# Optimization experiments

Measured on AMD Instinct MI355X. Metric: run time of the kernel, lower is better.

The kernel has to match this reference:

```python
import jax, jax.numpy as jnp
import numpy as np

# Module constants from init_kwargs
A, T, HID, H, EGO = 50, 50, 128, 32, 0
C = 4 * HID // H   # per-head out channels = 16
B = 32
NEG_SLOPE = 0.2    # PyG GATConv default negative_slope


def setup_inputs() -> dict:
    key = jax.random.key(0)
    k1, k2, k3, k4 = jax.random.split(key, 4)
    h = jax.random.normal(k1, (B, A, T, HID), dtype=jnp.float32)
    # GATConv params: lin.weight (H*C, HID), att_src/att_dst (H, C), bias (H*C,)
    W = jax.random.normal(k2, (H * C, HID), dtype=jnp.float32) * (1.0 / np.sqrt(HID))
    att_src = jax.random.normal(k3, (H, C), dtype=jnp.float32) * 0.1
    att_dst = jax.random.normal(k4, (H, C), dtype=jnp.float32) * 0.1
    bias = jnp.zeros((H * C,), dtype=jnp.float32)
    return {"h": h, "W": W, "att_src": att_src, "att_dst": att_dst, "bias": bias}


def reference(h, W, att_src, att_dst, bias):
    # h: (B, A, T, HID). Node id = t*A + a after permute, matching build_ego_star_edges.
    b = h.shape[0]
    x = jnp.transpose(h, (0, 2, 1, 3))                       # (B, T, A, HID)
    # Linear projection into heads: (B, T, A, H, C)
    xw = jnp.einsum('btad,hcd->btahc', x, W.reshape(H, C, HID))
    a_src = jnp.einsum('btahc,hc->btah', xw, att_src)        # per-node src logit
    a_dst = jnp.einsum('btahc,hc->btah', xw, att_dst)        # per-node dst logit

    # Star topology: every (t_src, a != EGO) node -> every (t_dst, EGO) node.
    ne = jnp.array([a for a in range(A) if a != EGO])        # (A-1,) non-ego agents
    S = T * (A - 1)                                          # neighbors per ego dst
    x_ne = xw[:, :, ne].reshape(b, S, H, C)                  # (B, S, H, C)
    a_src_ne = a_src[:, :, ne].reshape(b, S, H)              # (B, S, H)
    a_dst_ego = a_dst[:, :, EGO]                             # (B, T, H)

    # Per-edge attention logits, segment-softmax over the S neighbors of each dst.
    logits = jax.nn.leaky_relu(a_src_ne[:, None, :, :] + a_dst_ego[:, :, None, :],
                               negative_slope=NEG_SLOPE)     # (B, T, S, H)
    att = jax.nn.softmax(logits, axis=2)

    # Weighted aggregation: (B, T, H, C) -> flatten heads (concat=True)
    out_ego = jnp.einsum('btsh,bshc->bthc', att, x_ne).reshape(b, T, H * C)

    # Nodes with no incoming edges get zero aggregation; bias added to all.
    out = jnp.zeros((b, T, A, H * C), dtype=h.dtype).at[:, :, EGO].set(out_ego)
    out = out + bias
    return jnp.transpose(out, (0, 2, 1, 3))                  # (B, A, T, H*C)
```

## Files before the change

kernel.cpp:

```cpp
#include <hip/hip_runtime.h>
#include <math.h>

#define NA    50
#define NT    50
#define HIDK  128
#define NH    32
#define NC    16
#define NB    32
#define SAT   2500
#define NS    2450
#define NOUT  512

__global__ __launch_bounds__(256) void k_fill(const float* __restrict__ bias,
                                              float* __restrict__ out) {
  size_t i = (size_t)blockIdx.x * 256 + threadIdx.x;
  float4 b4 = ((const float4*)bias)[i & 127];
  ((float4*)out)[i] = b4;
}

__global__ __launch_bounds__(256) void k0_pq(const float* __restrict__ W,
                                             const float* __restrict__ att_src,
                                             const float* __restrict__ att_dst,
                                             float* __restrict__ PQ) {
  int g = blockIdx.x * 256 + threadIdx.x;
  int j = g >> 7, k = g & 127;
  int hh = j & 31;
  const float* att = (j < 32) ? att_src : att_dst;
  float acc = 0.f;
  #pragma unroll
  for (int c = 0; c < 16; ++c)
    acc = fmaf(att[hh * 16 + c], W[(size_t)(hh * 16 + c) * 128 + k], acc);
  PQ[g] = acc;
}

__global__ __launch_bounds__(256) void k1_ud(
    const float* __restrict__ X,
    const float* __restrict__ PQ,
    float* __restrict__ u,
    float* __restrict__ dv)
{
  __shared__ float Ast[32][68];
  __shared__ float Bst[32][68];
  const int tid = threadIdx.x;
  const int m0 = blockIdx.x * 64;
  const int ty = tid >> 4, tx = tid & 15;
  float acc[4][4] = {};
  const int sr = tid >> 3, sc = tid & 7;

  for (int kc = 0; kc < 128; kc += 32) {
    #pragma unroll
    for (int L = 0; L < 2; ++L) {
      int row = sr + L * 32;
      float4 v = *(const float4*)&X[(size_t)(m0 + row) * 128 + kc + sc * 4];
      Ast[sc*4+0][row] = v.x; Ast[sc*4+1][row] = v.y;
      Ast[sc*4+2][row] = v.z; Ast[sc*4+3][row] = v.w;
      float4 w = *(const float4*)&PQ[(size_t)row * 128 + kc + sc * 4];
      Bst[sc*4+0][row] = w.x; Bst[sc*4+1][row] = w.y;
      Bst[sc*4+2][row] = w.z; Bst[sc*4+3][row] = w.w;
    }
    __syncthreads();
    #pragma unroll
    for (int k = 0; k < 32; ++k) {
      float4 a4 = *(const float4*)&Ast[k][ty * 4];
      float4 b4 = *(const float4*)&Bst[k][tx * 4];
      float a[4] = {a4.x, a4.y, a4.z, a4.w};
      float bb[4] = {b4.x, b4.y, b4.z, b4.w};
      #pragma unroll
      for (int i = 0; i < 4; ++i)
        #pragma unroll
        for (int j = 0; j < 4; ++j)
          acc[i][j] = fmaf(a[i], bb[j], acc[i][j]);
    }
    __syncthreads();
  }

  #pragma unroll
  for (int i = 0; i < 4; ++i) {
    int m = m0 + ty * 4 + i;
    int b = m / SAT, s = m - b * SAT;
    #pragma unroll
    for (int jj = 0; jj < 4; ++jj) {
      int col = tx * 4 + jj;
      if (col < 32)
        u[(size_t)(b * 32 + col) * SAT + s] = acc[i][jj];
      else if (s < NT)
        dv[(size_t)(b * 32 + col - 32) * NT + s] = acc[i][jj];
    }
  }
}

#define LOADG(B_, g_) do {                                                  \
    _Pragma("unroll")                                                       \
    for (int j = 0; j < 4; ++j) {                                           \
      int idx_ = base + 2 * ((g_) * 4 + j);                                 \
      e##B_[j] = sE[idx_]; s##B_[j] = sIdx[idx_];                           \
    }                                                                       \
    _Pragma("unroll")                                                       \
    for (int j = 0; j < 4; ++j)                                             \
      x##B_[j] = *(const float4*)(xb + (size_t)s##B_[j] * HIDK);            \
  } while (0)

#define COMPG(B_) do {                                                      \
    _Pragma("unroll")                                                       \
    for (int j = 0; j < 4; ++j) {                                           \
      float2 ee = e##B_[j]; float4 xx = x##B_[j];                           \
      a1[0]=fmaf(ee.x,xx.x,a1[0]); a1[1]=fmaf(ee.x,xx.y,a1[1]);             \
      a1[2]=fmaf(ee.x,xx.z,a1[2]); a1[3]=fmaf(ee.x,xx.w,a1[3]);             \
      a2[0]=fmaf(ee.y,xx.x,a2[0]); a2[1]=fmaf(ee.y,xx.y,a2[1]);             \
      a2[2]=fmaf(ee.y,xx.z,a2[2]); a2[3]=fmaf(ee.y,xx.w,a2[3]);             \
      z1 += ee.x; z2 += ee.y;                                               \
    }                                                                       \
  } while (0)

__global__ __launch_bounds__(512, 4) void k2_attn(
    const float* __restrict__ X,
    const float* __restrict__ u,
    const float* __restrict__ dv,
    const float* __restrict__ W,
    const float* __restrict__ bias,
    float* __restrict__ out)
{
  const int id = blockIdx.x;
  const int b  = (id & 7) + 8 * (id >> 8);
  const int h  = (id >> 3) & 31;
  const int tid = threadIdx.x;

  __shared__ float Bb[2][51][129];
  __shared__ float2 sE[NS];
  __shared__ unsigned short sIdx[NS];
  __shared__ float sTheta[50], sD[50], sF1[50], sF2[50];
  __shared__ int   sRank[50];
  __shared__ int   offs[52];
  __shared__ int   offCur[51];
  __shared__ float red[8];
  __shared__ float sMaxU;

  float* sU = &Bb[0][0][0];
  unsigned short* sBeta = (unsigned short*)&Bb[1][0][0];

  const size_t bh = (size_t)b * 32 + h;
  const float* uP = u + bh * SAT + NT;
  for (int i = tid; i < NS; i += 512) sU[i] = uP[i];
  if (tid < 50) sD[tid] = dv[bh * NT + tid];
  if (tid < 51) offCur[tid] = 0;
  __syncthreads();

  float mx = -1e30f;
  for (int i = tid; i < NS; i += 512) mx = fmaxf(mx, sU[i]);
  #pragma unroll
  for (int o = 32; o; o >>= 1) mx = fmaxf(mx, __shfl_xor(mx, o));
  if ((tid & 63) == 0) red[tid >> 6] = mx;
  __syncthreads();
  if (tid == 0) {
    float m2 = red[0];
    #pragma unroll
    for (int k = 1; k < 8; ++k) m2 = fmaxf(m2, red[k]);
    sMaxU = m2;
  }
  __syncthreads();
  const float maxU = sMaxU;

  if (tid < 50) {
    float th = -sD[tid];
    int r = 0;
    for (int t2 = 0; t2 < 50; ++t2) {
      float th2 = -sD[t2];
      r += (th2 < th) || (th2 == th && t2 < tid);
    }
    sRank[tid] = r;
    sTheta[r] = th;
    float x = maxU + sD[tid];
    float L = (x >= 0.f) ? x : 0.2f * x;
    sF1[tid] = __expf(x - L);
    sF2[tid] = __expf(0.2f * x - L);
  }
  __syncthreads();

  for (int i = tid; i < NS; i += 512) {
    float uu = sU[i];
    int lo = 0, hi = 50;
    while (lo < hi) { int mid = (lo + hi) >> 1; if (sTheta[mid] <= uu) lo = mid + 1; else hi = mid; }
    sBeta[i] = (unsigned short)lo;
    atomicAdd(&offCur[lo], 1);
  }
  __syncthreads();
  if (tid == 0) {
    int run = 0;
    for (int k = 0; k < 51; ++k) { int c = offCur[k]; offs[k] = run; run += c; }
    offs[51] = run;
  }
  __syncthreads();
  if (tid < 51) offCur[tid] = offs[tid];
  __syncthreads();

  for (int i = tid; i < NS; i += 512) {
    float uu = sU[i];
    int beta = sBeta[i];
    int pos = atomicAdd(&offCur[beta], 1);
    sE[pos] = make_float2(__expf(uu - maxU), __expf(0.2f * (uu - maxU)));
    sIdx[pos] = (unsigned short)(i + NT);
  }
  __syncthreads();

  {
    const int wave = tid >> 6;
    const int lane = tid & 63;
    const int slot = lane >> 5;
    const int cq   = lane & 31;
    const float* xb = X + (size_t)b * SAT * HIDK + cq * 4;

    for (int seg = wave; seg < 51; seg += 8) {
      const int i0 = offs[seg], i1 = offs[seg + 1];
      const int base = i0 + slot;
      int np = i1 - base;
      np = (np > 0) ? ((np + 1) >> 1) : 0;
      const int G = np >> 2;

      float a1[4] = {0.f, 0.f, 0.f, 0.f};
      float a2[4] = {0.f, 0.f, 0.f, 0.f};
      float z1 = 0.f, z2 = 0.f;

      float2 eA[4], eB[4]; int sA[4], sB[4]; float4 xA[4], xB[4];
      int g = 0;
      if (G) LOADG(A, 0);
      while (g + 2 <= G) {
        LOADG(B, g + 1);
        COMPG(A);
        if (g + 2 < G) LOADG(A, g + 2);
        COMPG(B);
        g += 2;
      }
      if (g < G) COMPG(A);
      for (int k = G * 4; k < np; ++k) {
        int idx = base + 2 * k;
        float2 ee = sE[idx];
        int ss = sIdx[idx];
        float4 xx = *(const float4*)(xb + (size_t)ss * HIDK);
        a1[0]=fmaf(ee.x,xx.x,a1[0]); a1[1]=fmaf(ee.x,xx.y,a1[1]);
        a1[2]=fmaf(ee.x,xx.z,a1[2]); a1[3]=fmaf(ee.x,xx.w,a1[3]);
        a2[0]=fmaf(ee.y,xx.x,a2[0]); a2[1]=fmaf(ee.y,xx.y,a2[1]);
        a2[2]=fmaf(ee.y,xx.z,a2[2]); a2[3]=fmaf(ee.y,xx.w,a2[3]);
        z1 += ee.x; z2 += ee.y;
      }

      #pragma unroll
      for (int j = 0; j < 4; ++j) {
        a1[j] += __shfl_xor(a1[j], 32);
        a2[j] += __shfl_xor(a2[j], 32);
      }
      z1 += __shfl_xor(z1, 32);
      z2 += __shfl_xor(z2, 32);
      if (slot == 0) {
        #pragma unroll
        for (int j = 0; j < 4; ++j) {
          Bb[0][seg][cq * 4 + j] = a1[j];
          Bb[1][seg][cq * 4 + j] = a2[j];
        }
        if (cq == 0) { Bb[0][seg][128] = z1; Bb[1][seg][128] = z2; }
      }
    }
  }
  __syncthreads();

  float* WshT = (float*)sE;
  const float* Wh = W + (size_t)h * 16 * 128;
  for (int v = tid; v < 2048; v += 512) {
    int k = v >> 4, cout = v & 15;
    WshT[k * 16 + cout] = Wh[(size_t)cout * 128 + k];
  }
  for (int task = tid; task < 258; task += 512) {
    int which = task >= 129;
    int c = task - which * 129;
    if (which == 0) {
      float run = 0.f;
      for (int k = 50; k >= 0; --k) { float tmp = Bb[0][k][c]; Bb[0][k][c] = run; run += tmp; }
    } else {
      float run = 0.f;
      for (int k = 0; k <= 50; ++k) { run += Bb[1][k][c]; Bb[1][k][c] = run; }
    }
  }
  __syncthreads();

  for (int task = tid; task < NT * NC; task += 512) {
    int t = task >> 4, cout = task & 15;
    int r = sRank[t];
    float F1 = sF1[t], F2 = sF2[t];
    float z = F1 * Bb[0][r][128] + F2 * Bb[1][r][128];
    const float* b1r = &Bb[0][r][0];
    const float* b2r = &Bb[1][r][0];
    float n1 = 0.f, n2 = 0.f;
    #pragma unroll 4
    for (int c = 0; c < 128; ++c) {
      float w = WshT[c * 16 + cout];
      n1 = fmaf(b1r[c], w, n1);
      n2 = fmaf(b2r[c], w, n2);
    }
    out[((size_t)b * SAT + t) * NOUT + h * 16 + cout] =
        (F1 * n1 + F2 * n2) / z + bias[h * 16 + cout];
  }
}

extern "C" void kernel_launch(void* const* d_in, const int* in_sizes, int n_in,
                              void* d_out, int out_size, void* d_ws, size_t ws_size,
                              hipStream_t stream) {
  const float* X       = (const float*)d_in[0];
  const float* Wm      = (const float*)d_in[1];
  const float* att_src = (const float*)d_in[2];
  const float* att_dst = (const float*)d_in[3];
  const float* bias    = (const float*)d_in[4];
  float* out = (float*)d_out;

  float* PQ = (float*)d_ws;
  float* u  = PQ + 64 * 128;
  float* dv = u + (size_t)NB * NH * SAT;

  hipLaunchKernelGGL(k_fill, dim3(40000), dim3(256), 0, stream, bias, out);
  hipLaunchKernelGGL(k0_pq, dim3(32), dim3(256), 0, stream, Wm, att_src, att_dst, PQ);
  hipLaunchKernelGGL(k1_ud, dim3(1250), dim3(256), 0, stream, X, PQ, u, dv);
  hipLaunchKernelGGL(k2_attn, dim3(1024), dim3(512), 0, stream,
                     X, u, dv, Wm, bias, out);
}
```

Baseline: 318.7 us.

## Split attention kernel into gather and output stages, fold bias fill into output

Splits the big attention kernel into two. The gather kernel keeps only the sorted edge weights in LDS, which allows more resident blocks, and writes the partial sums plus per-head auxiliaries to workspace. A second kernel reloads them, runs the prefix scans and projection, and also writes the bias into the non-ego output rows, which replaces the separate full-output fill kernel. The cost is an extra global round-trip for the partial buffers, one more launch, and a repeated binary search.

New measurement: 682.7 us. 114% more time.

```diff
diff --git a/kernel.cpp b/kernel.cpp
--- a/kernel.cpp
+++ b/kernel.cpp
@@ -11,12 +11,10 @@
 #define NS    2450
 #define NOUT  512
 
-__global__ __launch_bounds__(256) void k_fill(const float* __restrict__ bias,
-                                              float* __restrict__ out) {
-  size_t i = (size_t)blockIdx.x * 256 + threadIdx.x;
-  float4 b4 = ((const float4*)bias)[i & 127];
-  ((float4*)out)[i] = b4;
-}
+#define SEGW   132
+#define WHICHW (51 * SEGW)
+#define BHW    (2 * WHICHW)
+#define AUXW   160
 
 __global__ __launch_bounds__(256) void k0_pq(const float* __restrict__ W,
                                              const float* __restrict__ att_src,
@@ -112,36 +110,32 @@
     }                                                                       \
   } while (0)
 
-__global__ __launch_bounds__(512, 4) void k2_attn(
+__global__ __launch_bounds__(512, 8) void k2a_gather(
     const float* __restrict__ X,
     const float* __restrict__ u,
     const float* __restrict__ dv,
-    const float* __restrict__ W,
-    const float* __restrict__ bias,
-    float* __restrict__ out)
+    float* __restrict__ Bpart,
+    float* __restrict__ aux)
 {
   const int id = blockIdx.x;
   const int b  = (id & 7) + 8 * (id >> 8);
   const int h  = (id >> 3) & 31;
   const int tid = threadIdx.x;
-
-  __shared__ float Bb[2][51][129];
+  const int bh = b * 32 + h;
+
   __shared__ float2 sE[NS];
+  __shared__ float  sU[NS];
   __shared__ unsigned short sIdx[NS];
-  __shared__ float sTheta[50], sD[50], sF1[50], sF2[50];
+  __shared__ float sTheta[50], sD[50];
   __shared__ int   sRank[50];
   __shared__ int   offs[52];
   __shared__ int   offCur[51];
   __shared__ float red[8];
   __shared__ float sMaxU;
 
-  float* sU = &Bb[0][0][0];
-  unsigned short* sBeta = (unsigned short*)&Bb[1][0][0];
-
-  const size_t bh = (size_t)b * 32 + h;
-  const float* uP = u + bh * SAT + NT;
+  const float* uP = u + (size_t)bh * SAT + NT;
   for (int i = tid; i < NS; i += 512) sU[i] = uP[i];
-  if (tid < 50) sD[tid] = dv[bh * NT + tid];
+  if (tid < 50) sD[tid] = dv[(size_t)bh * NT + tid];
   if (tid < 51) offCur[tid] = 0;
   __syncthreads();
 
@@ -171,8 +165,10 @@
     sTheta[r] = th;
     float x = maxU + sD[tid];
     float L = (x >= 0.f) ? x : 0.2f * x;
-    sF1[tid] = __expf(x - L);
-    sF2[tid] = __expf(0.2f * x - L);
+    float* ax = aux + (size_t)bh * AUXW;
+    ax[tid]       = __expf(x - L);
+    ax[50 + tid]  = __expf(0.2f * x - L);
+    ax[100 + tid] = (float)r;
   }
   __syncthreads();
 
@@ -180,7 +176,6 @@
     float uu = sU[i];
     int lo = 0, hi = 50;
     while (lo < hi) { int mid = (lo + hi) >> 1; if (sTheta[mid] <= uu) lo = mid + 1; else hi = mid; }
-    sBeta[i] = (unsigned short)lo;
     atomicAdd(&offCur[lo], 1);
   }
   __syncthreads();
@@ -195,8 +190,9 @@
 
   for (int i = tid; i < NS; i += 512) {
     float uu = sU[i];
-    int beta = sBeta[i];
-    int pos = atomicAdd(&offCur[beta], 1);
+    int lo = 0, hi = 50;
+    while (lo < hi) { int mid = (lo + hi) >> 1; if (sTheta[mid] <= uu) lo = mid + 1; else hi = mid; }
+    int pos = atomicAdd(&offCur[lo], 1);
     sE[pos] = make_float2(__expf(uu - maxU), __expf(0.2f * (uu - maxU)));
     sIdx[pos] = (unsigned short)(i + NT);
   }
@@ -208,6 +204,7 @@
     const int slot = lane >> 5;
     const int cq   = lane & 31;
     const float* xb = X + (size_t)b * SAT * HIDK + cq * 4;
+    float* bp = Bpart + (size_t)bh * BHW;
 
     for (int seg = wave; seg < 51; seg += 8) {
       const int i0 = offs[seg], i1 = offs[seg + 1];
@@ -251,24 +248,57 @@
       z1 += __shfl_xor(z1, 32);
       z2 += __shfl_xor(z2, 32);
       if (slot == 0) {
-        #pragma unroll
-        for (int j = 0; j < 4; ++j) {
-          Bb[0][seg][cq * 4 + j] = a1[j];
-          Bb[1][seg][cq * 4 + j] = a2[j];
+        float4 st1 = {a1[0], a1[1], a1[2], a1[3]};
+        float4 st2 = {a2[0], a2[1], a2[2], a2[3]};
+        *(float4*)&bp[seg * SEGW + cq * 4] = st1;
+        *(float4*)&bp[WHICHW + seg * SEGW + cq * 4] = st2;
+        if (cq == 0) {
+          bp[seg * SEGW + 128] = z1;
+          bp[WHICHW + seg * SEGW + 128] = z2;
         }
-        if (cq == 0) { Bb[0][seg][128] = z1; Bb[1][seg][128] = z2; }
       }
     }
   }
-  __syncthreads();
-
-  float* WshT = (float*)sE;
-  const float* Wh = W + (size_t)h * 16 * 128;
-  for (int v = tid; v < 2048; v += 512) {
-    int k = v >> 4, cout = v & 15;
-    WshT[k * 16 + cout] = Wh[(size_t)cout * 128 + k];
-  }
-  for (int task = tid; task < 258; task += 512) {
+}
+
+__global__ __launch_bounds__(256) void k2b_out(
+    const float* __restrict__ Bpart, const float* __restrict__ aux,
+    const float* __restrict__ W, const float* __restrict__ bias,
+    float* __restrict__ out)
+{
+  const int h = blockIdx.x & 31;
+  const int b = blockIdx.x >> 5;
+  const int bh = b * 32 + h;
+  const int tid = threadIdx.x;
+
+  __shared__ float Bb[2][51][SEGW];
+  __shared__ float WshT[128][16];
+  __shared__ float sF1[50], sF2[50];
+  __shared__ int   sRank[50];
+  __shared__ float sBias[512];
+
+  {
+    const float4* src = (const float4*)(Bpart + (size_t)bh * BHW);
+    float4* dst = (float4*)&Bb[0][0][0];
+    for (int i = tid; i < BHW / 4; i += 256) dst[i] = src[i];
+  }
+  if (tid < 50) {
+    const float* ax = aux + (size_t)bh * AUXW;
+    sF1[tid] = ax[tid];
+    sF2[tid] = ax[50 + tid];
+    sRank[tid] = (int)ax[100 + tid];
+  }
+  {
+    const float* Wh = W + (size_t)h * 16 * 128;
+    for (int v = tid; v < 2048; v += 256) {
+      int k = v >> 4, cout = v & 15;
+      WshT[k][cout] = Wh[(size_t)cout * 128 + k];
+    }
+    for (int i = tid; i < 512; i += 256) sBias[i] = bias[i];
+  }
+  __syncthreads();
+
+  for (int task = tid; task < 258; task += 256) {
     int which = task >= 129;
     int c = task - which * 129;
     if (which == 0) {
@@ -279,9 +309,21 @@
       for (int k = 0; k <= 50; ++k) { run += Bb[1][k][c]; Bb[1][k][c] = run; }
     }
   }
-  __syncthreads();
-
-  for (int task = tid; task < NT * NC; task += 512) {
+
+  {
+    const int r0 = (NS * h) >> 5;
+    const int r1 = (NS * (h + 1)) >> 5;
+    const int n = (r1 - r0) * 128;
+    float4* outp = (float4*)out;
+    const float4* bv = (const float4*)sBias;
+    for (int j = tid; j < n; j += 256) {
+      int row = r0 + (j >> 7), c4 = j & 127;
+      outp[((size_t)b * SAT + NT + row) * 128 + c4] = bv[c4];
+    }
+  }
+  __syncthreads();
+
+  for (int task = tid; task < NT * NC; task += 256) {
     int t = task >> 4, cout = task & 15;
     int r = sRank[t];
     float F1 = sF1[t], F2 = sF2[t];
@@ -291,12 +333,12 @@
     float n1 = 0.f, n2 = 0.f;
     #pragma unroll 4
     for (int c = 0; c < 128; ++c) {
-      float w = WshT[c * 16 + cout];
+      float w = WshT[c][cout];
       n1 = fmaf(b1r[c], w, n1);
       n2 = fmaf(b2r[c], w, n2);
     }
     out[((size_t)b * SAT + t) * NOUT + h * 16 + cout] =
-        (F1 * n1 + F2 * n2) / z + bias[h * 16 + cout];
+        (F1 * n1 + F2 * n2) / z + sBias[h * 16 + cout];
   }
 }
 
@@ -310,13 +352,14 @@
   const float* bias    = (const float*)d_in[4];
   float* out = (float*)d_out;
 
-  float* PQ = (float*)d_ws;
-  float* u  = PQ + 64 * 128;
-  float* dv = u + (size_t)NB * NH * SAT;
-
-  hipLaunchKernelGGL(k_fill, dim3(40000), dim3(256), 0, stream, bias, out);
+  float* PQ   = (float*)d_ws;
+  float* u    = PQ + 64 * 128;
+  float* dv   = u + (size_t)NB * NH * SAT;
+  float* aux  = dv + (size_t)NB * NH * NT;
+  float* Bpart = aux + (size_t)NB * NH * AUXW;
+
   hipLaunchKernelGGL(k0_pq, dim3(32), dim3(256), 0, stream, Wm, att_src, att_dst, PQ);
   hipLaunchKernelGGL(k1_ud, dim3(1250), dim3(256), 0, stream, X, PQ, u, dv);
-  hipLaunchKernelGGL(k2_attn, dim3(1024), dim3(512), 0, stream,
-                     X, u, dv, Wm, bias, out);
-}
+  hipLaunchKernelGGL(k2a_gather, dim3(1024), dim3(512), 0, stream, X, u, dv, Bpart, aux);
+  hipLaunchKernelGGL(k2b_out, dim3(1024), dim3(256), 0, stream, Bpart, aux, Wm, bias, out);
+}
```
